# Performance work log

Hardware: AMD Instinct MI355X
Metric: run time of the kernel (lower is better)

The kernel has to match this reference:

```python
import jax, jax.numpy as jnp
import numpy as np

B, C, V, L = 64, 32, 1024, 12
ORDER = 2


def setup_inputs() -> dict:
    key = jax.random.key(0)
    ks = jax.random.split(key, 6)
    x = jax.random.normal(ks[0], (B, C, V, L), dtype=jnp.float32)
    A1 = jax.random.uniform(ks[1], (V, V), dtype=jnp.float32)
    A2 = jax.random.uniform(ks[2], (V, V), dtype=jnp.float32)
    nodevec1 = jax.random.normal(ks[3], (V, 10), dtype=jnp.float32)
    nodevec2 = jax.random.normal(ks[4], (10, V), dtype=jnp.float32)
    c_cat = (ORDER * 3 + 1) * C  # 7*C = 224, matches gcn: (order*support_len+1)*c_in
    W_mlp = jax.random.normal(ks[5], (C, c_cat), dtype=jnp.float32) * 0.05
    b_mlp = jnp.zeros((C,), dtype=jnp.float32)
    return {"x": x, "A1": A1, "A2": A2, "nodevec1": nodevec1,
            "nodevec2": nodevec2, "W_mlp": W_mlp, "b_mlp": b_mlp}


def reference(x, A1, A2, nodevec1, nodevec2, W_mlp, b_mlp):
    # adaptive adjacency: softmax(relu(E1 @ E2), dim=1)  (graph-wavenet style)
    adp = jax.nn.softmax(jax.nn.relu(nodevec1 @ nodevec2), axis=1)  # [V, V]
    supports = (A1, A2, adp)
    # gcn.forward: multi-hop diffusion via nconv einsum, order=2
    out = [x]
    for a in supports:
        x1 = jnp.einsum('ncvl,vw->ncwl', x, a)   # hop 1
        out.append(x1)
        x2 = jnp.einsum('ncvl,vw->ncwl', x1, a)  # hop 2
        out.append(x2)
    h = jnp.concatenate(out, axis=1)             # [B, 7C, V, L]
    # linear: 1x1 Conv2d over channel dim (dropout is identity in eval)
    h = jnp.einsum('ncvl,oc->novl', h, W_mlp) + b_mlp[None, :, None, None]
    return h
```

## Files before the change

kernel.cpp:

```cpp
#include <hip/hip_runtime.h>
#include <hip/hip_bf16.h>


typedef __attribute__((ext_vector_type(8))) short short8;
typedef __attribute__((ext_vector_type(4))) float floatx4;

#define V_DIM 1024
#define L_DIM 12
#define B_DIM 64
#define C_DIM 32

__global__ __launch_bounds__(128) void adp_kernel(
    const float* __restrict__ nv1, const float* __restrict__ nv2,
    float* __restrict__ adp) {
  const int v = blockIdx.x, tid = threadIdx.x;
  float n1[10];
#pragma unroll
  for (int i = 0; i < 10; ++i) n1[i] = nv1[v * 10 + i];
  __shared__ float red[128];
  float e[8];
  float lmax = -1e30f;
#pragma unroll
  for (int j = 0; j < 8; ++j) {
    int w = tid + j * 128;
    float s = 0.f;
#pragma unroll
    for (int i = 0; i < 10; ++i) s += n1[i] * nv2[i * V_DIM + w];
    s = fmaxf(s, 0.f);
    e[j] = s;
    lmax = fmaxf(lmax, s);
  }
  red[tid] = lmax; __syncthreads();
  for (int s = 64; s > 0; s >>= 1) {
    if (tid < s) red[tid] = fmaxf(red[tid], red[tid + s]);
    __syncthreads();
  }
  float mx = red[0]; __syncthreads();
  float lsum = 0.f;
#pragma unroll
  for (int j = 0; j < 8; ++j) { e[j] = __expf(e[j] - mx); lsum += e[j]; }
  red[tid] = lsum; __syncthreads();
  for (int s = 64; s > 0; s >>= 1) {
    if (tid < s) red[tid] += red[tid + s];
    __syncthreads();
  }
  float inv = 1.f / red[0];
#pragma unroll
  for (int j = 0; j < 8; ++j) adp[(size_t)v * V_DIM + tid + j * 128] = e[j] * inv;
}

__global__ __launch_bounds__(256) void cast_transpose(
    const float* __restrict__ A1, const float* __restrict__ A2,
    const float* __restrict__ adp, __hip_bfloat16* __restrict__ As,
    __hip_bfloat16* __restrict__ BtCat) {
  const int z = blockIdx.z;
  const float* src = (z == 0) ? A1 : (z == 1) ? A2 : adp;
  __hip_bfloat16* sdst = As + (size_t)z * V_DIM * V_DIM;
  __hip_bfloat16* tdst = BtCat + (size_t)(2 * z) * V_DIM * V_DIM;
  __shared__ float tile[64][65];
  const int v0 = blockIdx.y * 64, w0 = blockIdx.x * 64;
  const int tc = threadIdx.x & 15, tr = threadIdx.x >> 4;
#pragma unroll
  for (int i = 0; i < 4; ++i) {
    int r = tr + i * 16;
    float4 val = *(const float4*)(src + (size_t)(v0 + r) * V_DIM + w0 + tc * 4);
    tile[r][tc * 4 + 0] = val.x; tile[r][tc * 4 + 1] = val.y;
    tile[r][tc * 4 + 2] = val.z; tile[r][tc * 4 + 3] = val.w;
    __hip_bfloat16* sp = sdst + (size_t)(v0 + r) * V_DIM + w0 + tc * 4;
    sp[0] = __float2bfloat16(val.x); sp[1] = __float2bfloat16(val.y);
    sp[2] = __float2bfloat16(val.z); sp[3] = __float2bfloat16(val.w);
  }
  __syncthreads();
#pragma unroll
  for (int i = 0; i < 4; ++i) {
    int r = tr + i * 16;
    __hip_bfloat16* tp = tdst + (size_t)(w0 + r) * V_DIM + v0 + tc * 4;
#pragma unroll
    for (int j = 0; j < 4; ++j) tp[j] = __float2bfloat16(tile[tc * 4 + j][r]);
  }
}

__global__ __launch_bounds__(256) void transpose_x_k(
    const float* __restrict__ x, __hip_bfloat16* __restrict__ xT) {
  const int bc = blockIdx.x;
  const int b = bc >> 5, c = bc & 31;
  __shared__ __align__(16) __hip_bfloat16 tile[V_DIM * L_DIM];
  const float4* src = (const float4*)(x + (size_t)bc * (V_DIM * L_DIM));
#pragma unroll
  for (int i = 0; i < 12; ++i) {
    int idx = threadIdx.x + i * 256;
    float4 v = src[idx];
    int e = idx * 4;
    tile[e + 0] = __float2bfloat16(v.x); tile[e + 1] = __float2bfloat16(v.y);
    tile[e + 2] = __float2bfloat16(v.z); tile[e + 3] = __float2bfloat16(v.w);
  }
  __syncthreads();
  for (int l = 0; l < L_DIM; ++l) {
    __hip_bfloat16* dst = xT + ((size_t)(b * L_DIM + l) * C_DIM + c) * V_DIM;
    for (int v = threadIdx.x; v < V_DIM; v += 256) dst[v] = tile[v * L_DIM + l];
  }
}

__device__ __forceinline__ void gll16(const __hip_bfloat16* g, __hip_bfloat16* l) {
  __builtin_amdgcn_global_load_lds(
      (const __attribute__((address_space(1))) void*)g,
      (__attribute__((address_space(3))) void*)l, 16, 0, 0);
}

template <int MODE>
__global__ __launch_bounds__(256) void gemm_bt(
    const __hip_bfloat16* __restrict__ Abase,
    const __hip_bfloat16* __restrict__ Btbase,
    __hip_bfloat16* __restrict__ Cbase, int M, int N, int K,
    long long aStride, long long bStride, long long cStride) {
  const __hip_bfloat16* A = Abase + (size_t)blockIdx.z * aStride;
  const __hip_bfloat16* Bt = Btbase + (size_t)blockIdx.z * bStride;
  __hip_bfloat16* C = Cbase + (size_t)blockIdx.z * cStride;
  __shared__ __align__(16) __hip_bfloat16 lA[128 * 64];
  __shared__ __align__(16) __hip_bfloat16 lB[128 * 64];
  const int tid = threadIdx.x;
  const int wv = tid >> 6, lane = tid & 63;
  const int wm = wv >> 1, wn = wv & 1;
  const int m0 = blockIdx.y * 128, n0 = blockIdx.x * 128;
  const int lrow = lane >> 3, lcol = lane & 7;
  const int gcol = lcol ^ (lrow & 7);
  const int fr = lane & 15, quad = lane >> 4;
  const int sw = fr & 7;

  floatx4 acc[4][4];
#pragma unroll
  for (int i = 0; i < 4; ++i)
#pragma unroll
    for (int j = 0; j < 4; ++j) acc[i][j] = (floatx4){0.f, 0.f, 0.f, 0.f};

  for (int kt = 0; kt < K; kt += 64) {
    __syncthreads();
#pragma unroll
    for (int i = 0; i < 4; ++i) {
      int r0 = (wv * 4 + i) * 8;
      gll16(A + (size_t)(m0 + r0 + lrow) * K + kt + gcol * 8, &lA[r0 * 64]);
      gll16(Bt + (size_t)(n0 + r0 + lrow) * K + kt + gcol * 8, &lB[r0 * 64]);
    }
    __syncthreads();
#pragma unroll
    for (int ks = 0; ks < 2; ++ks) {
      const int chunk = (ks * 4 + quad) ^ sw;
      short8 af[4], bfr[4];
#pragma unroll
      for (int t = 0; t < 4; ++t) {
        af[t] = *(const short8*)&lA[(wm * 64 + t * 16 + fr) * 64 + chunk * 8];
        bfr[t] = *(const short8*)&lB[(wn * 64 + t * 16 + fr) * 64 + chunk * 8];
      }
#pragma unroll
      for (int i = 0; i < 4; ++i)
#pragma unroll
        for (int j = 0; j < 4; ++j)
          acc[i][j] = __builtin_amdgcn_mfma_f32_16x16x32_bf16(af[i], bfr[j], acc[i][j], 0, 0, 0);
    }
  }
#pragma unroll
  for (int i = 0; i < 4; ++i) {
#pragma unroll
    for (int j = 0; j < 4; ++j) {
      int mb = m0 + wm * 64 + i * 16 + quad * 4;
      int n = n0 + wn * 64 + j * 16 + fr;
#pragma unroll
      for (int r = 0; r < 4; ++r) {
        int m = mb + r;
        float val = acc[i][j][r];
        size_t idx;
        if (MODE == 0) {
          idx = (size_t)m * N + n;
        } else {
          int c = m & 31, bl = m >> 5, k = n >> 10, w = n & 1023;
          idx = (((size_t)bl * 6 + k) * 32 + c) * 1024 + w;
        }
        C[idx] = __float2bfloat16(val);
      }
    }
  }
}

__global__ __launch_bounds__(256, 2) void gemm256(
    const __hip_bfloat16* __restrict__ A,
    const __hip_bfloat16* __restrict__ Bt,
    __hip_bfloat16* __restrict__ C) {
  constexpr int K = 1024;
  constexpr int NH = K / 32;
  __shared__ __align__(16) __hip_bfloat16 sA[3][256 * 32];
  __shared__ __align__(16) __hip_bfloat16 sB[3][128 * 32];
  const int tid = threadIdx.x;
  const int wv = tid >> 6, lane = tid & 63;
  const int wm = wv >> 1, wn = wv & 1;
  const int fr = lane & 15, quad = lane >> 4;
  const int rslot = (quad ^ ((fr >> 1) & 3)) << 3;
  const int aoff = (wm * 128 + fr) * 32 + rslot;
  const int boff = (wn * 64 + fr) * 32 + rslot;
  const int m0 = blockIdx.y * 256, n0 = blockIdx.x * 128;
  const int gch = ((lane & 3) ^ ((lane >> 3) & 3)) << 3;
  const __hip_bfloat16* Ag = A + (size_t)(m0 + wv * 16 + (lane >> 2)) * K + gch;
  const __hip_bfloat16* Bg = Bt + (size_t)(n0 + wv * 16 + (lane >> 2)) * K + gch;
  const int sb = (wv * 16) * 32;

  floatx4 acc[8][4];
#pragma unroll
  for (int i = 0; i < 8; ++i)
#pragma unroll
    for (int j = 0; j < 4; ++j) acc[i][j] = (floatx4){0.f, 0.f, 0.f, 0.f};

#define STAGE(hp, ur)                                                        \
  {                                                                          \
    _Pragma("unroll") for (int j = 0; j < 4; ++j)                            \
        gll16(Ag + (size_t)(j * 64) * K + (hp) * 32, &sA[ur][sb + j * 2048]);\
    _Pragma("unroll") for (int j = 0; j < 2; ++j)                            \
        gll16(Bg + (size_t)(j * 64) * K + (hp) * 32, &sB[ur][sb + j * 2048]);\
  }

  STAGE(0, 0)
  STAGE(1, 1)
  asm volatile("s_waitcnt vmcnt(6)" ::: "memory");
  __builtin_amdgcn_s_barrier();

  int u = 0, us = 2;
  for (int h = 0; h < NH; ++h) {
    short8 af[8], bf[4];
#pragma unroll
    for (int j = 0; j < 4; ++j) bf[j] = *(const short8*)&sB[u][boff + j * 512];
#pragma unroll
    for (int i = 0; i < 8; ++i) af[i] = *(const short8*)&sA[u][aoff + i * 512];
    if (h < NH - 2) STAGE(h + 2, us)
    __builtin_amdgcn_s_setprio(1);
#pragma unroll
    for (int i = 0; i < 8; ++i)
#pragma unroll
      for (int j = 0; j < 4; ++j)
        acc[i][j] = __builtin_amdgcn_mfma_f32_16x16x32_bf16(af[i], bf[j], acc[i][j], 0, 0, 0);
    __builtin_amdgcn_s_setprio(0);
    if (h < NH - 2) {
      asm volatile("s_waitcnt vmcnt(6)" ::: "memory");
    } else if (h == NH - 2) {
      asm volatile("s_waitcnt vmcnt(0)" ::: "memory");
    }
    __builtin_amdgcn_s_barrier();
    u = (u == 2) ? 0 : u + 1;
    us = (us == 2) ? 0 : us + 1;
  }
#undef STAGE

#pragma unroll
  for (int i = 0; i < 8; ++i) {
#pragma unroll
    for (int j = 0; j < 4; ++j) {
      int mb = m0 + wm * 128 + i * 16 + quad * 4;
      int n = n0 + wn * 64 + j * 16 + fr;
      int k = n >> 10, w = n & 1023;
#pragma unroll
      for (int r = 0; r < 4; ++r) {
        int m = mb + r;
        int c = m & 31, bl = m >> 5;
        size_t idx = (((size_t)bl * 6 + k) * 32 + c) * 1024 + w;
        C[idx] = __float2bfloat16(acc[i][j][r]);
      }
    }
  }
}

__global__ __launch_bounds__(256) void mix_kernel(
    const __hip_bfloat16* __restrict__ R, const __hip_bfloat16* __restrict__ xT,
    const float* __restrict__ W, const float* __restrict__ bias,
    float* __restrict__ out) {
  const int b = blockIdx.y, wt = blockIdx.x;
  const int tid = threadIdx.x;
  __shared__ __align__(16) __hip_bfloat16 tile[L_DIM * C_DIM * 64];
  __shared__ float Wl[7 * 32 * 32];
  for (int i = tid; i < 7168; i += 256) {
    int o = i / 224, cc = i - o * 224;
    Wl[cc * 32 + o] = W[i];
  }
  float acc[3][32];
#pragma unroll
  for (int pt = 0; pt < 3; ++pt)
#pragma unroll
    for (int o = 0; o < 32; ++o) acc[pt][o] = bias[o];
  int wloc[3], ll[3];
#pragma unroll
  for (int pt = 0; pt < 3; ++pt) {
    int wl = tid + pt * 256;
    wloc[pt] = wl / 12;
    ll[pt] = wl - wloc[pt] * 12;
  }
  const int w0 = wt * 64;
  for (int k = 0; k < 7; ++k) {
    __syncthreads();
    const __hip_bfloat16* srcp = (k < 6) ? R : xT;
    const int rps = (k < 6) ? 192 : 32;
    const int ko = (k < 6) ? k * 32 : 0;
#pragma unroll
    for (int i = 0; i < 24; ++i) {
      int q = tid + i * 256;
      int rr = q >> 4, ci = q & 15;
      int l = rr >> 5, c = rr & 31;
      size_t rowg = (size_t)(b * L_DIM + l) * rps + ko + c;
      *(ushort4*)&tile[rr * 64 + ci * 4] =
          *(const ushort4*)&srcp[rowg * V_DIM + w0 + ci * 4];
    }
    __syncthreads();
    const float* Wp = &Wl[((k < 6) ? (k + 1) : 0) * 1024];
    const int base0 = ll[0] * 2048 + wloc[0];
    const int base1 = ll[1] * 2048 + wloc[1];
    const int base2 = ll[2] * 2048 + wloc[2];
#pragma unroll 8
    for (int c = 0; c < 32; ++c) {
      float v0 = __bfloat162float(tile[base0 + c * 64]);
      float v1 = __bfloat162float(tile[base1 + c * 64]);
      float v2 = __bfloat162float(tile[base2 + c * 64]);
#pragma unroll
      for (int o = 0; o < 32; ++o) {
        float wv = Wp[c * 32 + o];
        acc[0][o] += wv * v0;
        acc[1][o] += wv * v1;
        acc[2][o] += wv * v2;
      }
    }
  }
  const size_t obase = (size_t)b * (32 * V_DIM * L_DIM) + (size_t)w0 * L_DIM;
#pragma unroll
  for (int o = 0; o < 32; ++o) {
    size_t base = obase + (size_t)o * (V_DIM * L_DIM);
    out[base + tid] = acc[0][o];
    out[base + tid + 256] = acc[1][o];
    out[base + tid + 512] = acc[2][o];
  }
}

extern "C" void kernel_launch(void* const* d_in, const int* in_sizes, int n_in,
                              void* d_out, int out_size, void* d_ws,
                              size_t ws_size, hipStream_t stream) {
  const float* x = (const float*)d_in[0];
  const float* A1 = (const float*)d_in[1];
  const float* A2 = (const float*)d_in[2];
  const float* nv1 = (const float*)d_in[3];
  const float* nv2 = (const float*)d_in[4];
  const float* W = (const float*)d_in[5];
  const float* bias = (const float*)d_in[6];
  float* out = (float*)d_out;

  char* ws = (char*)d_ws;
  __hip_bfloat16* R = (__hip_bfloat16*)(ws + 0);
  __hip_bfloat16* xT = (__hip_bfloat16*)(ws + 301989888ull);
  __hip_bfloat16* BtCat = (__hip_bfloat16*)(ws + 352321536ull);
  __hip_bfloat16* As = (__hip_bfloat16*)(ws + 364904448ull);
  float* adp = (float*)(ws + 371195904ull);

  adp_kernel<<<dim3(1024), dim3(128), 0, stream>>>(nv1, nv2, adp);
  cast_transpose<<<dim3(16, 16, 3), dim3(256), 0, stream>>>(A1, A2, adp, As, BtCat);
  gemm_bt<0><<<dim3(8, 8, 3), dim3(256), 0, stream>>>(
      BtCat, As, BtCat + 1048576ull, 1024, 1024, 1024,
      2097152ll, 1048576ll, 2097152ll);
  transpose_x_k<<<dim3(2048), dim3(256), 0, stream>>>(x, xT);
  gemm256<<<dim3(48, 96), dim3(256), 0, stream>>>(xT, BtCat, R);
  mix_kernel<<<dim3(16, 64), dim3(256), 0, stream>>>(R, xT, W, bias, out);
}
```

Baseline: 758.0 us.

## Replace scalar channel-mix kernel with MFMA GEMM on repacked diffusion outputs

The fp32 FMA mix_kernel is replaced by an MFMA-based kernel that uses split bf16 hi/lo weights to keep near-fp32 weight precision. The big GEMM's epilogue now writes its output in a channel-contiguous [b,l,w,192] layout with packed 4-element stores, so the mix can read contiguous K fragments. A small prep kernel reorders and splits W. The xT transpose store is also vectorised to ushort4. The xT operand in the mix is gathered with strided scalar loads, and the Whi/Wlo buffers reuse the workspace slot previously used by As.

```diff
diff --git a/kernel.cpp b/kernel.cpp
--- a/kernel.cpp
+++ b/kernel.cpp
@@ -95,9 +95,28 @@
     tile[e + 2] = __float2bfloat16(v.z); tile[e + 3] = __float2bfloat16(v.w);
   }
   __syncthreads();
+  const int v0 = threadIdx.x * 4;
   for (int l = 0; l < L_DIM; ++l) {
     __hip_bfloat16* dst = xT + ((size_t)(b * L_DIM + l) * C_DIM + c) * V_DIM;
-    for (int v = threadIdx.x; v < V_DIM; v += 256) dst[v] = tile[v * L_DIM + l];
+    ushort4 u;
+    u.x = *(const unsigned short*)&tile[(v0 + 0) * L_DIM + l];
+    u.y = *(const unsigned short*)&tile[(v0 + 1) * L_DIM + l];
+    u.z = *(const unsigned short*)&tile[(v0 + 2) * L_DIM + l];
+    u.w = *(const unsigned short*)&tile[(v0 + 3) * L_DIM + l];
+    *(ushort4*)&dst[v0] = u;
+  }
+}
+
+__global__ __launch_bounds__(256) void prep_w(
+    const float* __restrict__ W, __hip_bfloat16* __restrict__ Whi,
+    __hip_bfloat16* __restrict__ Wlo) {
+  for (int i = threadIdx.x; i < 32 * 224; i += 256) {
+    int o = i / 224, cc = i - o * 224;
+    int src = (cc < 192) ? (32 + cc) : (cc - 192);
+    float w = W[o * 224 + src];
+    __hip_bfloat16 h = __float2bfloat16(w);
+    Whi[i] = h;
+    Wlo[i] = __float2bfloat16(w - __bfloat162float(h));
   }
 }
 
@@ -167,15 +186,7 @@
 #pragma unroll
       for (int r = 0; r < 4; ++r) {
         int m = mb + r;
-        float val = acc[i][j][r];
-        size_t idx;
-        if (MODE == 0) {
-          idx = (size_t)m * N + n;
-        } else {
-          int c = m & 31, bl = m >> 5, k = n >> 10, w = n & 1023;
-          idx = (((size_t)bl * 6 + k) * 32 + c) * 1024 + w;
-        }
-        C[idx] = __float2bfloat16(val);
+        C[(size_t)m * N + n] = __float2bfloat16(acc[i][j][r]);
       }
     }
   }
@@ -184,7 +195,7 @@
 __global__ __launch_bounds__(256, 2) void gemm256(
     const __hip_bfloat16* __restrict__ A,
     const __hip_bfloat16* __restrict__ Bt,
-    __hip_bfloat16* __restrict__ C) {
+    __hip_bfloat16* __restrict__ Rp) {
   constexpr int K = 1024;
   constexpr int NH = K / 32;
   __shared__ __align__(16) __hip_bfloat16 sA[3][256 * 32];
@@ -254,83 +265,101 @@
       int mb = m0 + wm * 128 + i * 16 + quad * 4;
       int n = n0 + wn * 64 + j * 16 + fr;
       int k = n >> 10, w = n & 1023;
+      int bl = mb >> 5, c0 = mb & 31;
+      ushort4 pk;
+      unsigned short* pp = (unsigned short*)&pk;
 #pragma unroll
       for (int r = 0; r < 4; ++r) {
-        int m = mb + r;
-        int c = m & 31, bl = m >> 5;
-        size_t idx = (((size_t)bl * 6 + k) * 32 + c) * 1024 + w;
-        C[idx] = __float2bfloat16(acc[i][j][r]);
+        __hip_bfloat16 hv = __float2bfloat16(acc[i][j][r]);
+        pp[r] = *(unsigned short*)&hv;
       }
-    }
-  }
-}
-
-__global__ __launch_bounds__(256) void mix_kernel(
-    const __hip_bfloat16* __restrict__ R, const __hip_bfloat16* __restrict__ xT,
-    const float* __restrict__ W, const float* __restrict__ bias,
-    float* __restrict__ out) {
-  const int b = blockIdx.y, wt = blockIdx.x;
-  const int tid = threadIdx.x;
-  __shared__ __align__(16) __hip_bfloat16 tile[L_DIM * C_DIM * 64];
-  __shared__ float Wl[7 * 32 * 32];
-  for (int i = tid; i < 7168; i += 256) {
-    int o = i / 224, cc = i - o * 224;
-    Wl[cc * 32 + o] = W[i];
-  }
-  float acc[3][32];
-#pragma unroll
-  for (int pt = 0; pt < 3; ++pt)
-#pragma unroll
-    for (int o = 0; o < 32; ++o) acc[pt][o] = bias[o];
-  int wloc[3], ll[3];
-#pragma unroll
-  for (int pt = 0; pt < 3; ++pt) {
-    int wl = tid + pt * 256;
-    wloc[pt] = wl / 12;
-    ll[pt] = wl - wloc[pt] * 12;
-  }
-  const int w0 = wt * 64;
-  for (int k = 0; k < 7; ++k) {
-    __syncthreads();
-    const __hip_bfloat16* srcp = (k < 6) ? R : xT;
-    const int rps = (k < 6) ? 192 : 32;
-    const int ko = (k < 6) ? k * 32 : 0;
-#pragma unroll
-    for (int i = 0; i < 24; ++i) {
-      int q = tid + i * 256;
-      int rr = q >> 4, ci = q & 15;
-      int l = rr >> 5, c = rr & 31;
-      size_t rowg = (size_t)(b * L_DIM + l) * rps + ko + c;
-      *(ushort4*)&tile[rr * 64 + ci * 4] =
-          *(const ushort4*)&srcp[rowg * V_DIM + w0 + ci * 4];
-    }
-    __syncthreads();
-    const float* Wp = &Wl[((k < 6) ? (k + 1) : 0) * 1024];
-    const int base0 = ll[0] * 2048 + wloc[0];
-    const int base1 = ll[1] * 2048 + wloc[1];
-    const int base2 = ll[2] * 2048 + wloc[2];
-#pragma unroll 8
-    for (int c = 0; c < 32; ++c) {
-      float v0 = __bfloat162float(tile[base0 + c * 64]);
-      float v1 = __bfloat162float(tile[base1 + c * 64]);
-      float v2 = __bfloat162float(tile[base2 + c * 64]);
-#pragma unroll
-      for (int o = 0; o < 32; ++o) {
-        float wv = Wp[c * 32 + o];
-        acc[0][o] += wv * v0;
-        acc[1][o] += wv * v1;
-        acc[2][o] += wv * v2;
-      }
-    }
-  }
-  const size_t obase = (size_t)b * (32 * V_DIM * L_DIM) + (size_t)w0 * L_DIM;
-#pragma unroll
-  for (int o = 0; o < 32; ++o) {
-    size_t base = obase + (size_t)o * (V_DIM * L_DIM);
-    out[base + tid] = acc[0][o];
-    out[base + tid + 256] = acc[1][o];
-    out[base + tid + 512] = acc[2][o];
-  }
+      *(ushort4*)&Rp[((size_t)bl * 1024 + w) * 192 + k * 32 + c0] = pk;
+    }
+  }
+}
+
+__global__ __launch_bounds__(256) void mixmm(
+    const __hip_bfloat16* __restrict__ Rp, const __hip_bfloat16* __restrict__ xT,
+    const __hip_bfloat16* __restrict__ Whi, const __hip_bfloat16* __restrict__ Wlo,
+    const float* __restrict__ bias, float* __restrict__ out) {
+  const int b = blockIdx.y;
+  const int tid = threadIdx.x, wv = tid >> 6, lane = tid & 63;
+  const int fr = lane & 15, quad = lane >> 4;
+  const int n_base = blockIdx.x * 512 + wv * 128;
+
+  unsigned int rb[8], xb[8];
+#pragma unroll
+  for (int nf = 0; nf < 8; ++nf) {
+    int n = n_base + nf * 16 + fr;
+    int w = n / 12, l = n - w * 12;
+    int bl = b * L_DIM + l;
+    rb[nf] = ((unsigned)bl * 1024 + w) * 192 + quad * 8;
+    xb[nf] = (unsigned)bl * 32 * 1024 + w;
+  }
+  const int arow0 = fr * 224 + quad * 8;
+  const int arow1 = (16 + fr) * 224 + quad * 8;
+
+  floatx4 acc[2][8];
+#pragma unroll
+  for (int mt = 0; mt < 2; ++mt)
+#pragma unroll
+    for (int nf = 0; nf < 8; ++nf) acc[mt][nf] = (floatx4){0.f, 0.f, 0.f, 0.f};
+
+#pragma unroll
+  for (int ks = 0; ks < 6; ++ks) {
+    short8 bfr[8];
+#pragma unroll
+    for (int nf = 0; nf < 8; ++nf)
+      bfr[nf] = *(const short8*)&Rp[rb[nf] + ks * 32];
+    short8 a0h = *(const short8*)&Whi[arow0 + ks * 32];
+    short8 a1h = *(const short8*)&Whi[arow1 + ks * 32];
+    short8 a0l = *(const short8*)&Wlo[arow0 + ks * 32];
+    short8 a1l = *(const short8*)&Wlo[arow1 + ks * 32];
+#pragma unroll
+    for (int nf = 0; nf < 8; ++nf) {
+      acc[0][nf] = __builtin_amdgcn_mfma_f32_16x16x32_bf16(a0h, bfr[nf], acc[0][nf], 0, 0, 0);
+      acc[1][nf] = __builtin_amdgcn_mfma_f32_16x16x32_bf16(a1h, bfr[nf], acc[1][nf], 0, 0, 0);
+      acc[0][nf] = __builtin_amdgcn_mfma_f32_16x16x32_bf16(a0l, bfr[nf], acc[0][nf], 0, 0, 0);
+      acc[1][nf] = __builtin_amdgcn_mfma_f32_16x16x32_bf16(a1l, bfr[nf], acc[1][nf], 0, 0, 0);
+    }
+  }
+  {
+    short8 bfr[8];
+#pragma unroll
+    for (int nf = 0; nf < 8; ++nf) {
+      short8 v;
+#pragma unroll
+      for (int e = 0; e < 8; ++e)
+        v[e] = *(const short*)&xT[(size_t)xb[nf] + (unsigned)(quad * 8 + e) * 1024];
+      bfr[nf] = v;
+    }
+    short8 a0h = *(const short8*)&Whi[arow0 + 192];
+    short8 a1h = *(const short8*)&Whi[arow1 + 192];
+    short8 a0l = *(const short8*)&Wlo[arow0 + 192];
+    short8 a1l = *(const short8*)&Wlo[arow1 + 192];
+#pragma unroll
+    for (int nf = 0; nf < 8; ++nf) {
+      acc[0][nf] = __builtin_amdgcn_mfma_f32_16x16x32_bf16(a0h, bfr[nf], acc[0][nf], 0, 0, 0);
+      acc[1][nf] = __builtin_amdgcn_mfma_f32_16x16x32_bf16(a1h, bfr[nf], acc[1][nf], 0, 0, 0);
+      acc[0][nf] = __builtin_amdgcn_mfma_f32_16x16x32_bf16(a0l, bfr[nf], acc[0][nf], 0, 0, 0);
+      acc[1][nf] = __builtin_amdgcn_mfma_f32_16x16x32_bf16(a1l, bfr[nf], acc[1][nf], 0, 0, 0);
+    }
+  }
+  float bv[2][4];
+#pragma unroll
+  for (int mt = 0; mt < 2; ++mt)
+#pragma unroll
+    for (int r = 0; r < 4; ++r) bv[mt][r] = bias[mt * 16 + quad * 4 + r];
+#pragma unroll
+  for (int mt = 0; mt < 2; ++mt)
+#pragma unroll
+    for (int nf = 0; nf < 8; ++nf) {
+      float* op = out + ((size_t)b * 32 + mt * 16 + quad * 4) * 12288 +
+                  n_base + nf * 16 + fr;
+#pragma unroll
+      for (int r = 0; r < 4; ++r)
+        op[(size_t)r * 12288] = acc[mt][nf][r] + bv[mt][r];
+    }
 }
 
 extern "C" void kernel_launch(void* const* d_in, const int* in_sizes, int n_in,
@@ -346,18 +375,21 @@
   float* out = (float*)d_out;
 
   char* ws = (char*)d_ws;
-  __hip_bfloat16* R = (__hip_bfloat16*)(ws + 0);
+  __hip_bfloat16* Rp = (__hip_bfloat16*)(ws + 0);
   __hip_bfloat16* xT = (__hip_bfloat16*)(ws + 301989888ull);
   __hip_bfloat16* BtCat = (__hip_bfloat16*)(ws + 352321536ull);
   __hip_bfloat16* As = (__hip_bfloat16*)(ws + 364904448ull);
   float* adp = (float*)(ws + 371195904ull);
+  __hip_bfloat16* Whi = (__hip_bfloat16*)(ws + 364904448ull);
+  __hip_bfloat16* Wlo = Whi + 32 * 224;
 
   adp_kernel<<<dim3(1024), dim3(128), 0, stream>>>(nv1, nv2, adp);
   cast_transpose<<<dim3(16, 16, 3), dim3(256), 0, stream>>>(A1, A2, adp, As, BtCat);
   gemm_bt<0><<<dim3(8, 8, 3), dim3(256), 0, stream>>>(
       BtCat, As, BtCat + 1048576ull, 1024, 1024, 1024,
       2097152ll, 1048576ll, 2097152ll);
+  prep_w<<<dim3(1), dim3(256), 0, stream>>>(W, Whi, Wlo);
   transpose_x_k<<<dim3(2048), dim3(256), 0, stream>>>(x, xT);
-  gemm256<<<dim3(48, 96), dim3(256), 0, stream>>>(xT, BtCat, R);
-  mix_kernel<<<dim3(16, 64), dim3(256), 0, stream>>>(R, xT, W, bias, out);
-}
+  gemm256<<<dim3(48, 96), dim3(256), 0, stream>>>(xT, BtCat, Rp);
+  mixmm<<<dim3(24, 64), dim3(256), 0, stream>>>(Rp, xT, Whi, Wlo, bias, out);
+}
```

New measurement: 712.3 us. 1.06x faster.
